# Kernel optimization log

Hardware: AMD Instinct MI355X
Metric: run time of the kernel (lower is better)

The kernel has to match this reference:

```python
import jax, jax.numpy as jnp
import numpy as np

DIM = 256
L = 16            # block_size (query rows per leaf block)
H = 8             # num_heads
D = DIM // H      # head_dim = 32
KC = L + 1        # key count: L leaf nodes + 1 block (mean) node, layout '16x17'
B = 2
N = 32768         # multiple of L -> no padding path
NB = N // L       # 2048 blocks
SCALE = D ** -0.5


def setup_inputs() -> dict:
    key = jax.random.key(0)
    ks = jax.random.split(key, 8)
    x = jax.random.normal(ks[0], (B, N, DIM), jnp.float32)
    attn_mask = jax.random.randint(ks[1], (NB, L, KC), 0, 2, dtype=jnp.int32)
    ar = jnp.arange(L)
    attn_mask = attn_mask.at[:, ar, ar].set(1)  # self always visible -> no all-masked rows
    edge_feats = jax.random.normal(ks[2], (NB, L, KC, 4), jnp.float32)
    s = DIM ** -0.5
    Wqkv = jax.random.normal(ks[3], (3 * DIM, DIM), jnp.float32) * s
    bqkv = jnp.zeros((3 * DIM,), jnp.float32)
    Wproj = jax.random.normal(ks[4], (DIM, DIM), jnp.float32) * s
    bproj = jnp.zeros((DIM,), jnp.float32)
    Wgate = jax.random.normal(ks[5], (H, 4), jnp.float32) * 0.01  # nn.init.normal_(std=0.01)
    bgate = jnp.zeros((H,), jnp.float32)
    return {"x": x, "attn_mask": attn_mask, "edge_feats": edge_feats,
            "Wqkv": Wqkv, "bqkv": bqkv, "Wproj": Wproj, "bproj": bproj,
            "Wgate": Wgate, "bgate": bgate}


def reference(x, attn_mask, edge_feats, Wqkv, bqkv, Wproj, bproj, Wgate, bgate):
    # x: [B, N, C] -> blocks [B, NB, L, C]
    x_blk = x.reshape(B, NB, L, DIM)
    block_node = x_blk.mean(axis=2, keepdims=True)           # virtual block node
    kv = jnp.concatenate([x_blk, block_node], axis=2)         # [B, NB, KC, C]

    # qkv projections (slice of the fused Linear; rows are independent so math is identical)
    q = x_blk @ Wqkv[:DIM].T + bqkv[:DIM]
    k = kv @ Wqkv[DIM:2 * DIM].T + bqkv[DIM:2 * DIM]
    v = kv @ Wqkv[2 * DIM:].T + bqkv[2 * DIM:]
    q = q.reshape(B, NB, L, H, D)
    k = k.reshape(B, NB, KC, H, D)
    v = v.reshape(B, NB, KC, H, D)

    scores = jnp.einsum('bnqhd,bnkhd->bnqkh', q, k) * SCALE   # [B, NB, L, KC, H]

    # physics bias: zero out + set channel 3 = 1 for block node column and self (diagonal)
    ar = jnp.arange(L)
    unit = jnp.array([0.0, 0.0, 0.0, 1.0], edge_feats.dtype)
    bias = edge_feats.at[:, :, L, :].set(unit)                # block-node column
    bias = bias.at[:, ar, ar, :].set(unit)                    # self bias on diagonal
    bias = jnp.broadcast_to(bias[None], (B, NB, L, KC, 4))    # expand over batch

    scores = scores + bias[..., 3:4]

    mask0 = (attn_mask[None] == 0)[..., None]                 # [1, NB, L, KC, 1]
    scores = jnp.where(mask0, -jnp.inf, scores)
    attn = jax.nn.softmax(scores, axis=3)

    gate = jnp.einsum('bnqkf,hf->bnqkh', bias, Wgate) + bgate  # edge-conditioned gate
    gate = jnp.where(mask0, 0.0, gate)

    combined = attn + gate
    out = jnp.einsum('bnqkh,bnkhd->bnqhd', combined, v).reshape(B, N, DIM)
    return out @ Wproj.T + bproj
```

## Files before the change

kernel.cpp:

```cpp
#include <hip/hip_runtime.h>
#include <cstdint>
#include <cstddef>

#define B_SZ 2
#define N_SEQ 32768
#define NB 2048
#define HD 32
#define LQ 16
#define KCNT 17
#define M_ROWS 65536
#define SCALE_F 0.17677669529663687f

typedef __attribute__((ext_vector_type(8))) short sv8;
typedef __attribute__((ext_vector_type(4))) short sv4;
typedef __attribute__((ext_vector_type(4))) float f4;

__device__ __forceinline__ short f2bf(float f) {
  unsigned u = __builtin_bit_cast(unsigned, f);
  u = (u + 0x7FFFu + ((u >> 16) & 1u)) >> 16;
  return (short)u;
}
__device__ __forceinline__ float bf2f(short s) {
  unsigned u = ((unsigned)(unsigned short)s) << 16;
  return __builtin_bit_cast(float, u);
}
__device__ __forceinline__ void gload16(const void* g, void* l) {
  __builtin_amdgcn_global_load_lds(
      (const __attribute__((address_space(1))) unsigned int*)g,
      (__attribute__((address_space(3))) unsigned int*)l, 16, 0, 0);
}
__device__ __forceinline__ f4 mfma16(sv8 a, sv8 b, f4 c) {
  return __builtin_amdgcn_mfma_f32_16x16x32_bf16(a, b, c, 0, 0, 0);
}

__global__ __launch_bounds__(256) void cast_all(
    const float* __restrict__ x, const float* __restrict__ wq,
    const float* __restrict__ wp, short* __restrict__ X1,
    short* __restrict__ W1, short* __restrict__ WP1) {
  const int i = blockIdx.x * 256 + threadIdx.x;
  const float* src;
  short* dst;
  int off;
  if (i < 4194304) { src = x; dst = X1; off = i; }
  else if (i < 4194304 + 49152) { src = wq; dst = W1; off = i - 4194304; }
  else if (i < 4194304 + 49152 + 16384) { src = wp; dst = WP1; off = i - 4194304 - 49152; }
  else return;
  float4 v = ((const float4*)src)[off];
  sv4 h = {f2bf(v.x), f2bf(v.y), f2bf(v.z), f2bf(v.w)};
  *(sv4*)&dst[(size_t)off * 4] = h;
}

__global__ __launch_bounds__(256) void gemm_bf_qkv(
    const short* __restrict__ A1, const short* __restrict__ B1,
    const float* __restrict__ bias, short* __restrict__ Qbf,
    short* __restrict__ Kbf, short* __restrict__ Vbf) {
  __shared__ __align__(16) short LB[2][2][128][32];
  const int tid = threadIdx.x;
  const int w = tid >> 6, l = tid & 63;
  const int wm = w >> 1, wn = w & 1;
  const int bid = blockIdx.x;
  const int chunkc = (6 * 512) >> 3;
  const int lbid = (bid & 7) * chunkc + (bid >> 3);
  const int nti = lbid % 6, mti = lbid / 6;
  const int m0 = mti * 128, n0 = nti * 128;
  const int lr = l >> 2, lc = (l & 3) * 8;
  const int fr = l & 15, kg = (l >> 4) * 8;
  f4 acc[4][4] = {};
#pragma unroll
  for (int i = 0; i < 2; ++i) {
    const int row = w * 32 + i * 16;
    gload16(A1 + (size_t)(m0 + row + lr) * 256 + lc, (void*)&LB[0][0][row][0]);
    gload16(B1 + (size_t)(n0 + row + lr) * 256 + lc, (void*)&LB[0][1][row][0]);
  }
  asm volatile("s_waitcnt vmcnt(0)" ::: "memory");
  __builtin_amdgcn_s_barrier();
  int cur = 0;
  for (int s = 0; s < 8; ++s) {
    if (s < 7) {
      const int sk = (s + 1) * 32;
#pragma unroll
      for (int i = 0; i < 2; ++i) {
        const int row = w * 32 + i * 16;
        gload16(A1 + (size_t)(m0 + row + lr) * 256 + sk + lc,
                (void*)&LB[cur ^ 1][0][row][0]);
        gload16(B1 + (size_t)(n0 + row + lr) * 256 + sk + lc,
                (void*)&LB[cur ^ 1][1][row][0]);
      }
    }
    if (s > 0) {
      if (s < 7) asm volatile("s_waitcnt vmcnt(4)" ::: "memory");
      else asm volatile("s_waitcnt vmcnt(0)" ::: "memory");
      __builtin_amdgcn_s_barrier();
    }
    sv8 fa[4], fb[4];
#pragma unroll
    for (int t = 0; t < 4; ++t) {
      fa[t] = *(const sv8*)&LB[cur][0][wm * 64 + t * 16 + fr][kg];
      fb[t] = *(const sv8*)&LB[cur][1][wn * 64 + t * 16 + fr][kg];
    }
#pragma unroll
    for (int mt = 0; mt < 4; ++mt)
#pragma unroll
      for (int nt2 = 0; nt2 < 4; ++nt2)
        acc[mt][nt2] = mfma16(fa[mt], fb[nt2], acc[mt][nt2]);
    asm volatile("s_waitcnt lgkmcnt(0)" ::: "memory");
    __builtin_amdgcn_s_barrier();
    cur ^= 1;
  }
  short* Lout = &LB[0][0][0][0];
  const int r0 = (l >> 4) * 4;
#pragma unroll
  for (int mt = 0; mt < 4; ++mt)
#pragma unroll
    for (int nt2 = 0; nt2 < 4; ++nt2) {
      const int n = wn * 64 + nt2 * 16 + fr;
      const float bv = bias[n0 + n];
#pragma unroll
      for (int j = 0; j < 4; ++j) {
        const int m = wm * 64 + mt * 16 + r0 + j;
        Lout[m * 128 + (n ^ ((m & 7) << 3))] = f2bf(acc[mt][nt2][j] + bv);
      }
    }
  __builtin_amdgcn_s_barrier();
  short* dst = (nti < 2) ? Qbf : ((nti < 4) ? Kbf : Vbf);
  const int nnb = (nti & 1) * 128;
  const int rrow = tid >> 4, seg = (tid & 15) * 8;
#pragma unroll
  for (int p = 0; p < 8; ++p) {
    const int row = p * 16 + rrow;
    sv8 v = *(const sv8*)&Lout[row * 128 + (seg ^ ((row & 7) << 3))];
    *(sv8*)&dst[(size_t)(m0 + row) * 256 + nnb + seg] = v;
  }
}

__global__ __launch_bounds__(256) void gemm_proj1(
    const short* __restrict__ A1, const short* __restrict__ B1,
    const float* __restrict__ bias, float* __restrict__ C) {
  __shared__ __align__(16) short Ahs[2][128][32];
  __shared__ __align__(16) short Bhs[2][128][32];
  const int tid = threadIdx.x;
  const int w = tid >> 6, l = tid & 63;
  const int wm = w >> 1, wn = w & 1;
  const int bid = blockIdx.x;
  const int chunkc = (2 * 512) >> 3;
  const int lbid = (bid & 7) * chunkc + (bid >> 3);
  const int nti = lbid % 2, mti = lbid / 2;
  const int m0 = mti * 128, n0 = nti * 128;
  const int lr = l >> 2, lc = (l & 3) * 8;
  const int fr = l & 15, kg = (l >> 4) * 8;
  f4 acc[4][4] = {};
#pragma unroll
  for (int i = 0; i < 2; ++i) {
    const int row = w * 32 + i * 16;
    gload16(A1 + (size_t)(m0 + row + lr) * 256 + lc, (void*)&Ahs[0][row][0]);
    gload16(B1 + (size_t)(n0 + row + lr) * 256 + lc, (void*)&Bhs[0][row][0]);
  }
  asm volatile("s_waitcnt vmcnt(0)" ::: "memory");
  __builtin_amdgcn_s_barrier();
  int cur = 0;
  for (int s = 0; s < 8; ++s) {
    if (s < 7) {
      const int sk = (s + 1) * 32;
#pragma unroll
      for (int i = 0; i < 2; ++i) {
        const int row = w * 32 + i * 16;
        gload16(A1 + (size_t)(m0 + row + lr) * 256 + sk + lc,
                (void*)&Ahs[cur ^ 1][row][0]);
        gload16(B1 + (size_t)(n0 + row + lr) * 256 + sk + lc,
                (void*)&Bhs[cur ^ 1][row][0]);
      }
    }
    if (s > 0) {
      if (s < 7) asm volatile("s_waitcnt vmcnt(4)" ::: "memory");
      else asm volatile("s_waitcnt vmcnt(0)" ::: "memory");
      __builtin_amdgcn_s_barrier();
    }
    sv8 fa[4], fb[4];
#pragma unroll
    for (int t = 0; t < 4; ++t) {
      fa[t] = *(const sv8*)&Ahs[cur][wm * 64 + t * 16 + fr][kg];
      fb[t] = *(const sv8*)&Bhs[cur][wn * 64 + t * 16 + fr][kg];
    }
#pragma unroll
    for (int mt = 0; mt < 4; ++mt)
#pragma unroll
      for (int nt2 = 0; nt2 < 4; ++nt2)
        acc[mt][nt2] = mfma16(fa[mt], fb[nt2], acc[mt][nt2]);
    asm volatile("s_waitcnt lgkmcnt(0)" ::: "memory");
    __builtin_amdgcn_s_barrier();
    cur ^= 1;
  }
  const int r0 = (l >> 4) * 4;
#pragma unroll
  for (int mt = 0; mt < 4; ++mt)
#pragma unroll
    for (int nt2 = 0; nt2 < 4; ++nt2) {
      const int n = n0 + wn * 64 + nt2 * 16 + fr;
      const float bv = bias[n];
      const size_t mb = (size_t)(m0 + wm * 64 + mt * 16 + r0);
#pragma unroll
      for (int j = 0; j < 4; ++j) C[(mb + j) * 256 + n] = acc[mt][nt2][j] + bv;
    }
}

__global__ __launch_bounds__(256, 5) void attn_v7(
    const short* __restrict__ Qb, const short* __restrict__ Kb,
    const short* __restrict__ Vb, const int* __restrict__ amask,
    const float* __restrict__ efeat, const float* __restrict__ Wgate,
    const float* __restrict__ bgate, short* __restrict__ AO) {
  __shared__ __align__(16) short Kl[16 * 264];
  __shared__ __align__(16) short Vl[16 * 264];
  __shared__ __align__(16) short Ol[16 * 264];
  __shared__ float4 Es[LQ * KCNT];
  __shared__ int Ms[LQ * KCNT];

  const int tid = threadIdx.x, g = blockIdx.x;
  const int b = g >> 11, nb = g & (NB - 1);
  const size_t tok0 = (size_t)(b * N_SEQ + nb * LQ);
  const int w = tid >> 6, l = tid & 63;
  const int ln = l & 15, lg = l >> 4;
  const f4 fzero = {0.f, 0.f, 0.f, 0.f};

  sv8 qf[2];
#pragma unroll
  for (int hh = 0; hh < 2; ++hh) {
    const int h = w * 2 + hh;
    qf[hh] = *(const sv8*)(Qb + (tok0 + ln) * 256 + h * 32 + lg * 8);
  }

#pragma unroll
  for (int i = 0; i < 2; ++i) {
    const int f = tid + i * 256;
    const int t = f >> 5, c8 = (f & 31) * 8;
    *(sv8*)&Kl[t * 264 + c8] = *(const sv8*)(Kb + (tok0 + t) * 256 + c8);
    *(sv8*)&Vl[t * 264 + c8] = *(const sv8*)(Vb + (tok0 + t) * 256 + c8);
  }
  {
    const float4* esrc = (const float4*)(efeat + (size_t)nb * LQ * KCNT * 4);
    const int* msrc = amask + (size_t)nb * LQ * KCNT;
    Es[tid] = esrc[tid];
    Ms[tid] = msrc[tid];
    if (tid < LQ * KCNT - 256) {
      Es[256 + tid] = esrc[256 + tid];
      Ms[256 + tid] = msrc[256 + tid];
    }
  }
  __syncthreads();

  const int q = ln;
#pragma unroll
  for (int hh = 0; hh < 2; ++hh) {
    const int h = w * 2 + hh;
    sv8 ka = *(const sv8*)&Kl[ln * 264 + h * 32 + lg * 8];
    f4 sr = mfma16(ka, qf[hh], fzero);

    const float wg0 = Wgate[h * 4], wg1 = Wgate[h * 4 + 1];
    const float wg2 = Wgate[h * 4 + 2], wg3 = Wgate[h * 4 + 3];
    const float bg = bgate[h];

    float rs = sr[0] + sr[1] + sr[2] + sr[3];
    rs += __shfl_xor(rs, 16);
    rs += __shfl_xor(rs, 32);

    float s_[4], gt_[4];
    int vis_[4];
#pragma unroll
    for (int j = 0; j < 4; ++j) {
      const int kc = lg * 4 + j;
      float e0, e1, e2, e3;
      if (kc == q) { e0 = e1 = e2 = 0.f; e3 = 1.f; }
      else { float4 e = Es[q * KCNT + kc]; e0 = e.x; e1 = e.y; e2 = e.z; e3 = e.w; }
      const int m = Ms[q * KCNT + kc];
      vis_[j] = m;
      s_[j] = sr[j] * SCALE_F + e3;
      gt_[j] = m ? (e0 * wg0 + e1 * wg1 + e2 * wg2 + e3 * wg3 + bg) : 0.f;
    }
    const int m16 = Ms[q * KCNT + 16];
    const float s16 = rs * 0.0625f * SCALE_F + 1.0f;

    float mx = -1e30f;
#pragma unroll
    for (int j = 0; j < 4; ++j)
      if (vis_[j]) mx = fmaxf(mx, s_[j]);
    mx = fmaxf(mx, __shfl_xor(mx, 16));
    mx = fmaxf(mx, __shfl_xor(mx, 32));
    if (m16) mx = fmaxf(mx, s16);

    float p_[4], den = 0.f;
#pragma unroll
    for (int j = 0; j < 4; ++j) {
      p_[j] = vis_[j] ? __expf(s_[j] - mx) : 0.f;
      den += p_[j];
    }
    den += __shfl_xor(den, 16);
    den += __shfl_xor(den, 32);
    const float p16 = m16 ? __expf(s16 - mx) : 0.f;
    den += p16;
    const float inv = 1.f / den;
    const float gt16 = m16 ? (wg3 + bg) : 0.f;
    const float cb16 = (p16 * inv + gt16) * 0.0625f;
    float pc[4];
#pragma unroll
    for (int j = 0; j < 4; ++j) pc[j] = p_[j] * inv + gt_[j] + cb16;

    sv8 pa;
#pragma unroll
    for (int e = 0; e < 8; ++e) {
      const int kc = lg * 8 + e;
      const int src = ((kc >> 2) << 4) | q;
      const float v0 = __shfl(pc[e & 3], src);
      pa[e] = (kc < 16) ? f2bf(v0) : (short)0;
    }

#pragma unroll
    for (int t = 0; t < 2; ++t) {
      sv8 vb;
#pragma unroll
      for (int e = 0; e < 8; ++e) {
        const int vr = (lg * 8 + e) & 15;
        vb[e] = Vl[vr * 264 + h * 32 + t * 16 + ln];
      }
      f4 oacc = mfma16(pa, vb, fzero);
#pragma unroll
      for (int j = 0; j < 4; ++j)
        Ol[(lg * 4 + j) * 264 + h * 32 + t * 16 + ln] = f2bf(oacc[j]);
    }
  }
  __syncthreads();

#pragma unroll
  for (int i = 0; i < 2; ++i) {
    const int f = tid + i * 256;
    const int t = f >> 5, c8 = (f & 31) * 8;
    *(sv8*)(AO + (tok0 + t) * 256 + c8) = *(const sv8*)&Ol[t * 264 + c8];
  }
}

extern "C" void kernel_launch(void* const* d_in, const int* in_sizes, int n_in,
                              void* d_out, int out_size, void* d_ws, size_t ws_size,
                              hipStream_t stream) {
  const float* x = (const float*)d_in[0];
  const int* amask = (const int*)d_in[1];
  const float* efeat = (const float*)d_in[2];
  const float* Wqkv = (const float*)d_in[3];
  const float* bqkv = (const float*)d_in[4];
  const float* Wproj = (const float*)d_in[5];
  const float* bproj = (const float*)d_in[6];
  const float* Wgate = (const float*)d_in[7];
  const float* bgate = (const float*)d_in[8];
  float* out = (float*)d_out;

  char* ws = (char*)d_ws;
  const size_t QB_SZ = (size_t)M_ROWS * 256 * 2;
  const size_t W1_SZ = (size_t)768 * 256 * 2;
  const size_t WP1_SZ = (size_t)256 * 256 * 2;
  if (ws_size < 5 * QB_SZ + W1_SZ + WP1_SZ) return;

  short* X1 = (short*)ws;
  short* Qbf = (short*)(ws + QB_SZ);
  short* Kbf = (short*)(ws + 2 * QB_SZ);
  short* Vbf = (short*)(ws + 3 * QB_SZ);
  short* AOh = (short*)(ws + 4 * QB_SZ);
  short* W1 = (short*)(ws + 5 * QB_SZ);
  short* WP1 = (short*)(ws + 5 * QB_SZ + W1_SZ);

  const int total_f4 = 4194304 + 49152 + 16384;
  cast_all<<<dim3((total_f4 + 255) / 256), 256, 0, stream>>>(x, Wqkv, Wproj,
                                                             X1, W1, WP1);
  gemm_bf_qkv<<<dim3(6 * 512), 256, 0, stream>>>(X1, W1, bqkv, Qbf, Kbf, Vbf);
  attn_v7<<<dim3(B_SZ * NB), 256, 0, stream>>>(Qbf, Kbf, Vbf, amask, efeat,
                                               Wgate, bgate, AOh);
  gemm_proj1<<<dim3(2 * 512), 256, 0, stream>>>(AOh, WP1, bproj, out);
}
```

Baseline: 122.8 us.

## Fuse output projection into attention kernel, dropping the separate proj GEMM

The attention kernel now multiplies its 16x256 bf16 output tile in shared memory directly by Wproj, loading B fragments straight from global memory. It adds the bias and writes fp32 output through a reused shared buffer. This removes the bf16 attention-output round trip through global memory and one kernel launch. In exchange, every block re-reads the full 128KB Wproj from global/L2 without LDS reuse, and occupancy is lowered to 4 blocks per SM.

```diff
diff --git a/kernel.cpp b/kernel.cpp
--- a/kernel.cpp
+++ b/kernel.cpp
@@ -133,86 +133,19 @@
   }
 }
 
-__global__ __launch_bounds__(256) void gemm_proj1(
-    const short* __restrict__ A1, const short* __restrict__ B1,
-    const float* __restrict__ bias, float* __restrict__ C) {
-  __shared__ __align__(16) short Ahs[2][128][32];
-  __shared__ __align__(16) short Bhs[2][128][32];
-  const int tid = threadIdx.x;
-  const int w = tid >> 6, l = tid & 63;
-  const int wm = w >> 1, wn = w & 1;
-  const int bid = blockIdx.x;
-  const int chunkc = (2 * 512) >> 3;
-  const int lbid = (bid & 7) * chunkc + (bid >> 3);
-  const int nti = lbid % 2, mti = lbid / 2;
-  const int m0 = mti * 128, n0 = nti * 128;
-  const int lr = l >> 2, lc = (l & 3) * 8;
-  const int fr = l & 15, kg = (l >> 4) * 8;
-  f4 acc[4][4] = {};
-#pragma unroll
-  for (int i = 0; i < 2; ++i) {
-    const int row = w * 32 + i * 16;
-    gload16(A1 + (size_t)(m0 + row + lr) * 256 + lc, (void*)&Ahs[0][row][0]);
-    gload16(B1 + (size_t)(n0 + row + lr) * 256 + lc, (void*)&Bhs[0][row][0]);
-  }
-  asm volatile("s_waitcnt vmcnt(0)" ::: "memory");
-  __builtin_amdgcn_s_barrier();
-  int cur = 0;
-  for (int s = 0; s < 8; ++s) {
-    if (s < 7) {
-      const int sk = (s + 1) * 32;
-#pragma unroll
-      for (int i = 0; i < 2; ++i) {
-        const int row = w * 32 + i * 16;
-        gload16(A1 + (size_t)(m0 + row + lr) * 256 + sk + lc,
-                (void*)&Ahs[cur ^ 1][row][0]);
-        gload16(B1 + (size_t)(n0 + row + lr) * 256 + sk + lc,
-                (void*)&Bhs[cur ^ 1][row][0]);
-      }
-    }
-    if (s > 0) {
-      if (s < 7) asm volatile("s_waitcnt vmcnt(4)" ::: "memory");
-      else asm volatile("s_waitcnt vmcnt(0)" ::: "memory");
-      __builtin_amdgcn_s_barrier();
-    }
-    sv8 fa[4], fb[4];
-#pragma unroll
-    for (int t = 0; t < 4; ++t) {
-      fa[t] = *(const sv8*)&Ahs[cur][wm * 64 + t * 16 + fr][kg];
-      fb[t] = *(const sv8*)&Bhs[cur][wn * 64 + t * 16 + fr][kg];
-    }
-#pragma unroll
-    for (int mt = 0; mt < 4; ++mt)
-#pragma unroll
-      for (int nt2 = 0; nt2 < 4; ++nt2)
-        acc[mt][nt2] = mfma16(fa[mt], fb[nt2], acc[mt][nt2]);
-    asm volatile("s_waitcnt lgkmcnt(0)" ::: "memory");
-    __builtin_amdgcn_s_barrier();
-    cur ^= 1;
-  }
-  const int r0 = (l >> 4) * 4;
-#pragma unroll
-  for (int mt = 0; mt < 4; ++mt)
-#pragma unroll
-    for (int nt2 = 0; nt2 < 4; ++nt2) {
-      const int n = n0 + wn * 64 + nt2 * 16 + fr;
-      const float bv = bias[n];
-      const size_t mb = (size_t)(m0 + wm * 64 + mt * 16 + r0);
-#pragma unroll
-      for (int j = 0; j < 4; ++j) C[(mb + j) * 256 + n] = acc[mt][nt2][j] + bv;
-    }
-}
-
-__global__ __launch_bounds__(256, 5) void attn_v7(
+__global__ __launch_bounds__(256, 4) void attn_proj(
     const short* __restrict__ Qb, const short* __restrict__ Kb,
     const short* __restrict__ Vb, const int* __restrict__ amask,
     const float* __restrict__ efeat, const float* __restrict__ Wgate,
-    const float* __restrict__ bgate, short* __restrict__ AO) {
-  __shared__ __align__(16) short Kl[16 * 264];
-  __shared__ __align__(16) short Vl[16 * 264];
-  __shared__ __align__(16) short Ol[16 * 264];
+    const float* __restrict__ bgate, const short* __restrict__ WP1,
+    const float* __restrict__ bproj, float* __restrict__ out) {
+  __shared__ __align__(16) short Buf[12672];
   __shared__ float4 Es[LQ * KCNT];
   __shared__ int Ms[LQ * KCNT];
+  short* Kl = Buf;
+  short* Vl = Buf + 4224;
+  short* Ol = Buf + 8448;
+  float* Fl = (float*)Buf;
 
   const int tid = threadIdx.x, g = blockIdx.x;
   const int b = g >> 11, nb = g & (NB - 1);
@@ -328,11 +261,30 @@
   }
   __syncthreads();
 
-#pragma unroll
-  for (int i = 0; i < 2; ++i) {
-    const int f = tid + i * 256;
-    const int t = f >> 5, c8 = (f & 31) * 8;
-    *(sv8*)(AO + (tok0 + t) * 256 + c8) = *(const sv8*)&Ol[t * 264 + c8];
+  f4 pacc[4] = {};
+#pragma unroll
+  for (int kc8 = 0; kc8 < 8; ++kc8) {
+    sv8 a = *(const sv8*)&Ol[ln * 264 + kc8 * 32 + lg * 8];
+#pragma unroll
+    for (int nt = 0; nt < 4; ++nt) {
+      sv8 bfr = *(const sv8*)(WP1 + (size_t)(w * 64 + nt * 16 + ln) * 256 +
+                              kc8 * 32 + lg * 8);
+      pacc[nt] = mfma16(a, bfr, pacc[nt]);
+    }
+  }
+#pragma unroll
+  for (int nt = 0; nt < 4; ++nt) {
+    const int n = w * 64 + nt * 16 + ln;
+    const float bv = bproj[n];
+#pragma unroll
+    for (int j = 0; j < 4; ++j) Fl[(lg * 4 + j) * 260 + n] = pacc[nt][j] + bv;
+  }
+  __syncthreads();
+#pragma unroll
+  for (int i = 0; i < 4; ++i) {
+    const int idx = tid + i * 256;
+    const int row = idx >> 6, c4 = (idx & 63) * 4;
+    *(float4*)(out + (tok0 + row) * 256 + c4) = *(const float4*)&Fl[row * 260 + c4];
   }
 }
 
@@ -354,21 +306,19 @@
   const size_t QB_SZ = (size_t)M_ROWS * 256 * 2;
   const size_t W1_SZ = (size_t)768 * 256 * 2;
   const size_t WP1_SZ = (size_t)256 * 256 * 2;
-  if (ws_size < 5 * QB_SZ + W1_SZ + WP1_SZ) return;
+  if (ws_size < 4 * QB_SZ + W1_SZ + WP1_SZ) return;
 
   short* X1 = (short*)ws;
   short* Qbf = (short*)(ws + QB_SZ);
   short* Kbf = (short*)(ws + 2 * QB_SZ);
   short* Vbf = (short*)(ws + 3 * QB_SZ);
-  short* AOh = (short*)(ws + 4 * QB_SZ);
-  short* W1 = (short*)(ws + 5 * QB_SZ);
-  short* WP1 = (short*)(ws + 5 * QB_SZ + W1_SZ);
+  short* W1 = (short*)(ws + 4 * QB_SZ);
+  short* WP1 = (short*)(ws + 4 * QB_SZ + W1_SZ);
 
   const int total_f4 = 4194304 + 49152 + 16384;
   cast_all<<<dim3((total_f4 + 255) / 256), 256, 0, stream>>>(x, Wqkv, Wproj,
                                                              X1, W1, WP1);
   gemm_bf_qkv<<<dim3(6 * 512), 256, 0, stream>>>(X1, W1, bqkv, Qbf, Kbf, Vbf);
-  attn_v7<<<dim3(B_SZ * NB), 256, 0, stream>>>(Qbf, Kbf, Vbf, amask, efeat,
-                                               Wgate, bgate, AOh);
-  gemm_proj1<<<dim3(2 * 512), 256, 0, stream>>>(AOh, WP1, bproj, out);
-}
+  attn_proj<<<dim3(B_SZ * NB), 256, 0, stream>>>(Qbf, Kbf, Vbf, amask, efeat,
+                                                 Wgate, bgate, WP1, bproj, out);
+}
```

Result: slower. 147.0 us (+19.7%).

## Enlarge QKV GEMM tile to 256x128 with 512-thread blocks

Applied to the files above, without the earlier changes.

The QKV projection GEMM now uses 256-row M tiles with 8 waves per block, and each staged B tile is shared by twice as many A rows. This halves the block count and the repeated loading of weight tiles, and changes the LDS load pattern and waitcnt accounting to match. The epilogue writes output in two halves through LDS with extra barriers, since the staging buffer only holds 128 rows at a time. Larger blocks may lower occupancy and raise barrier cost.

```diff
diff --git a/kernel.cpp b/kernel.cpp
--- a/kernel.cpp
+++ b/kernel.cpp
@@ -50,28 +50,28 @@
   *(sv4*)&dst[(size_t)off * 4] = h;
 }
 
-__global__ __launch_bounds__(256) void gemm_bf_qkv(
+__global__ __launch_bounds__(512) void gemm_bf_qkv(
     const short* __restrict__ A1, const short* __restrict__ B1,
     const float* __restrict__ bias, short* __restrict__ Qbf,
     short* __restrict__ Kbf, short* __restrict__ Vbf) {
-  __shared__ __align__(16) short LB[2][2][128][32];
+  __shared__ __align__(16) short As[2][256][32];
+  __shared__ __align__(16) short Bs[2][128][32];
   const int tid = threadIdx.x;
   const int w = tid >> 6, l = tid & 63;
   const int wm = w >> 1, wn = w & 1;
   const int bid = blockIdx.x;
-  const int chunkc = (6 * 512) >> 3;
+  const int chunkc = (6 * 256) >> 3;
   const int lbid = (bid & 7) * chunkc + (bid >> 3);
   const int nti = lbid % 6, mti = lbid / 6;
-  const int m0 = mti * 128, n0 = nti * 128;
+  const int m0 = mti * 256, n0 = nti * 128;
   const int lr = l >> 2, lc = (l & 3) * 8;
   const int fr = l & 15, kg = (l >> 4) * 8;
   f4 acc[4][4] = {};
 #pragma unroll
-  for (int i = 0; i < 2; ++i) {
-    const int row = w * 32 + i * 16;
-    gload16(A1 + (size_t)(m0 + row + lr) * 256 + lc, (void*)&LB[0][0][row][0]);
-    gload16(B1 + (size_t)(n0 + row + lr) * 256 + lc, (void*)&LB[0][1][row][0]);
-  }
+  for (int i = 0; i < 2; ++i)
+    gload16(A1 + (size_t)(m0 + i * 128 + w * 16 + lr) * 256 + lc,
+            (void*)&As[0][i * 128 + w * 16][0]);
+  gload16(B1 + (size_t)(n0 + w * 16 + lr) * 256 + lc, (void*)&Bs[0][w * 16][0]);
   asm volatile("s_waitcnt vmcnt(0)" ::: "memory");
   __builtin_amdgcn_s_barrier();
   int cur = 0;
@@ -79,24 +79,22 @@
     if (s < 7) {
       const int sk = (s + 1) * 32;
 #pragma unroll
-      for (int i = 0; i < 2; ++i) {
-        const int row = w * 32 + i * 16;
-        gload16(A1 + (size_t)(m0 + row + lr) * 256 + sk + lc,
-                (void*)&LB[cur ^ 1][0][row][0]);
-        gload16(B1 + (size_t)(n0 + row + lr) * 256 + sk + lc,
-                (void*)&LB[cur ^ 1][1][row][0]);
-      }
+      for (int i = 0; i < 2; ++i)
+        gload16(A1 + (size_t)(m0 + i * 128 + w * 16 + lr) * 256 + sk + lc,
+                (void*)&As[cur ^ 1][i * 128 + w * 16][0]);
+      gload16(B1 + (size_t)(n0 + w * 16 + lr) * 256 + sk + lc,
+              (void*)&Bs[cur ^ 1][w * 16][0]);
     }
     if (s > 0) {
-      if (s < 7) asm volatile("s_waitcnt vmcnt(4)" ::: "memory");
+      if (s < 7) asm volatile("s_waitcnt vmcnt(3)" ::: "memory");
       else asm volatile("s_waitcnt vmcnt(0)" ::: "memory");
       __builtin_amdgcn_s_barrier();
     }
     sv8 fa[4], fb[4];
 #pragma unroll
     for (int t = 0; t < 4; ++t) {
-      fa[t] = *(const sv8*)&LB[cur][0][wm * 64 + t * 16 + fr][kg];
-      fb[t] = *(const sv8*)&LB[cur][1][wn * 64 + t * 16 + fr][kg];
+      fa[t] = *(const sv8*)&As[cur][wm * 64 + t * 16 + fr][kg];
+      fb[t] = *(const sv8*)&Bs[cur][wn * 64 + t * 16 + fr][kg];
     }
 #pragma unroll
     for (int mt = 0; mt < 4; ++mt)
@@ -107,29 +105,36 @@
     __builtin_amdgcn_s_barrier();
     cur ^= 1;
   }
-  short* Lout = &LB[0][0][0][0];
-  const int r0 = (l >> 4) * 4;
-#pragma unroll
-  for (int mt = 0; mt < 4; ++mt)
-#pragma unroll
-    for (int nt2 = 0; nt2 < 4; ++nt2) {
-      const int n = wn * 64 + nt2 * 16 + fr;
-      const float bv = bias[n0 + n];
-#pragma unroll
-      for (int j = 0; j < 4; ++j) {
-        const int m = wm * 64 + mt * 16 + r0 + j;
-        Lout[m * 128 + (n ^ ((m & 7) << 3))] = f2bf(acc[mt][nt2][j] + bv);
-      }
-    }
-  __builtin_amdgcn_s_barrier();
+  short* Lout = (short*)As;
   short* dst = (nti < 2) ? Qbf : ((nti < 4) ? Kbf : Vbf);
   const int nnb = (nti & 1) * 128;
+  const int r0 = (l >> 4) * 4;
   const int rrow = tid >> 4, seg = (tid & 15) * 8;
 #pragma unroll
-  for (int p = 0; p < 8; ++p) {
-    const int row = p * 16 + rrow;
-    sv8 v = *(const sv8*)&Lout[row * 128 + (seg ^ ((row & 7) << 3))];
-    *(sv8*)&dst[(size_t)(m0 + row) * 256 + nnb + seg] = v;
+  for (int half = 0; half < 2; ++half) {
+    if ((wm >> 1) == half) {
+      const int mb = (wm & 1) * 64;
+#pragma unroll
+      for (int mt = 0; mt < 4; ++mt)
+#pragma unroll
+        for (int nt2 = 0; nt2 < 4; ++nt2) {
+          const int n = wn * 64 + nt2 * 16 + fr;
+          const float bv = bias[n0 + n];
+#pragma unroll
+          for (int j = 0; j < 4; ++j) {
+            const int m = mb + mt * 16 + r0 + j;
+            Lout[m * 128 + (n ^ ((m & 7) << 3))] = f2bf(acc[mt][nt2][j] + bv);
+          }
+        }
+    }
+    __builtin_amdgcn_s_barrier();
+#pragma unroll
+    for (int p = 0; p < 4; ++p) {
+      const int row = p * 32 + rrow;
+      sv8 v = *(const sv8*)&Lout[row * 128 + (seg ^ ((row & 7) << 3))];
+      *(sv8*)&dst[(size_t)(m0 + half * 128 + row) * 256 + nnb + seg] = v;
+    }
+    __builtin_amdgcn_s_barrier();
   }
 }
 
@@ -367,7 +372,7 @@
   const int total_f4 = 4194304 + 49152 + 16384;
   cast_all<<<dim3((total_f4 + 255) / 256), 256, 0, stream>>>(x, Wqkv, Wproj,
                                                              X1, W1, WP1);
-  gemm_bf_qkv<<<dim3(6 * 512), 256, 0, stream>>>(X1, W1, bqkv, Qbf, Kbf, Vbf);
+  gemm_bf_qkv<<<dim3(6 * 256), 512, 0, stream>>>(X1, W1, bqkv, Qbf, Kbf, Vbf);
   attn_v7<<<dim3(B_SZ * NB), 256, 0, stream>>>(Qbf, Kbf, Vbf, amask, efeat,
                                                Wgate, bgate, AOh);
   gemm_proj1<<<dim3(2 * 512), 256, 0, stream>>>(AOh, WP1, bproj, out);
```

Result: slower. 139.1 us (+13.2%).
